# Optimization experiments

Hardware: AMD Instinct MI355X
Metric: run time of the kernel (lower is better)

## Reference

```python
import jax, jax.numpy as jnp
import numpy as np

N = 50000      # nodes
E = 800000     # edges
D_DISC = 64
D_CONT = 13    # per-slice continuous features (39/3)
EMB = 256
HID = 512
SLOPE = 0.01   # torch leaky_relu default


def lrelu(x):
    return jax.nn.leaky_relu(x, SLOPE)


def gcn_conv(x, W, b, src, dst, n):
    """PyG GCNConv with add_self_loops=True (self loops appended by caller),
    symmetric normalization D^-1/2 A D^-1/2, bias."""
    x = x @ W                                   # [N, EMB]
    ones = jnp.ones(src.shape[0], x.dtype)
    deg = jax.ops.segment_sum(ones, dst, num_segments=n)   # in-degree incl self loop
    dinv = jax.lax.rsqrt(jnp.maximum(deg, 1e-12))
    norm = dinv[src] * dinv[dst]                # [E+N]
    out = jax.ops.segment_sum(x[src] * norm[:, None], dst, num_segments=n)
    return out + b


def setup_inputs() -> dict:
    key = jax.random.key(0)
    ks = jax.random.split(key, 24)
    def lin(k, fan_in, fan_out):
        bound = 1.0 / np.sqrt(fan_in)
        k1, k2 = jax.random.split(k)
        W = jax.random.uniform(k1, (fan_in, fan_out), jnp.float32, -bound, bound)
        b = jax.random.uniform(k2, (fan_out,), jnp.float32, -bound, bound)
        return W, b
    Wd, bd = lin(ks[0], D_DISC, EMB)
    Wc1, bc1 = lin(ks[1], D_CONT, EMB)
    Wc2, bc2 = lin(ks[2], D_CONT, EMB)
    Wg0, bg0 = lin(ks[3], D_DISC, EMB)
    Wg1, bg1 = lin(ks[4], EMB, EMB)
    Wg2, bg2 = lin(ks[5], EMB, EMB)
    Wf, bf = lin(ks[6], 4 * EMB, HID)
    Wl1, bl1 = lin(ks[7], HID, HID // 2)
    Wl2, bl2 = lin(ks[8], HID // 2, 1)
    discrete_x = jax.random.normal(ks[9], (N, D_DISC), jnp.float32)
    continous_x = jax.random.normal(ks[10], (N, 3 * D_CONT), jnp.float32)
    edge_index = jax.random.randint(ks[11], (2, E), 0, N, jnp.int64)
    return {
        'discrete_x': discrete_x, 'continous_x': continous_x,
        'Wd': Wd, 'bd': bd, 'Wc1': Wc1, 'bc1': bc1, 'Wc2': Wc2, 'bc2': bc2,
        'Wg0': Wg0, 'bg0': bg0, 'Wg1': Wg1, 'bg1': bg1, 'Wg2': Wg2, 'bg2': bg2,
        'Wf': Wf, 'bf': bf, 'Wl1': Wl1, 'bl1': bl1, 'Wl2': Wl2, 'bl2': bl2,
        'edge_index': edge_index,
    }


def reference(discrete_x, continous_x, Wd, bd, Wc1, bc1, Wc2, bc2,
              Wg0, bg0, Wg1, bg1, Wg2, bg2, Wf, bf, Wl1, bl1, Wl2, bl2,
              edge_index):
    n = discrete_x.shape[0]
    loop = jnp.arange(n, dtype=edge_index.dtype)
    src = jnp.concatenate([edge_index[0], loop])
    dst = jnp.concatenate([edge_index[1], loop])

    x_d = lrelu(discrete_x @ Wd + bd)
    x_c1 = lrelu(continous_x[:, :13] @ Wc1 + bc1)
    x_c2 = lrelu(continous_x[:, 13:26] @ Wc2 + bc2)
    x_g = lrelu(discrete_x @ Wg0 + bg0)
    x_g = lrelu(gcn_conv(x_g, Wg1, bg1, src, dst, n))
    x_g = lrelu(gcn_conv(x_g, Wg2, bg2, src, dst, n))

    h_ci = lrelu(jnp.concatenate([x_d, x_c1, x_c2, x_g], axis=1) @ Wf + bf)
    s = lrelu(h_ci @ Wl1 + bl1)
    # dropout: eval mode (training=False) -> identity
    s_ci = jax.nn.sigmoid((s @ Wl2 + bl2)).squeeze()
    return (s_ci, s_ci, s_ci, h_ci, h_ci)
```

## Files before the change

kernel.cpp:

```cpp
#include <hip/hip_runtime.h>
#include <math.h>

#define NNODES 50000
#define NEDGES 800000
#define EMB 256
#define HID 512


typedef __bf16 bf16x8 __attribute__((ext_vector_type(8)));
typedef float f32x4 __attribute__((ext_vector_type(4)));
typedef unsigned short us4v __attribute__((ext_vector_type(4)));
typedef unsigned short us8v __attribute__((ext_vector_type(8)));

__device__ __forceinline__ unsigned short f2bf(float x) {
    unsigned int u = __float_as_uint(x);
    u += 0x7FFF + ((u >> 16) & 1);
    return (unsigned short)(u >> 16);
}

__device__ __forceinline__ f32x4 mfma_bf16(us8v a, us8v b, f32x4 c) {
    return __builtin_amdgcn_mfma_f32_16x16x32_bf16(
        __builtin_bit_cast(bf16x8, a), __builtin_bit_cast(bf16x8, b), c, 0, 0, 0);
}

__device__ __forceinline__ void gl16(const unsigned short* g, unsigned short* l) {
    __builtin_amdgcn_global_load_lds(
        (const __attribute__((address_space(1))) unsigned int*)g,
        (__attribute__((address_space(3))) unsigned int*)l, 16, 0, 0);
}

__global__ void wsplit(const float* __restrict__ W, int K, int N,
                       unsigned short* __restrict__ th, unsigned short* __restrict__ tl)
{
    int idx = blockIdx.x * 256 + threadIdx.x;
    if (idx >= K * N) return;
    int n = idx / K, k = idx - n * K;
    float x = W[(size_t)k * N + n];
    unsigned short h = f2bf(x);
    float hf = __uint_as_float((unsigned int)h << 16);
    th[idx] = h;
    tl[idx] = f2bf(x - hf);
}

__global__ void xsplit(const float* __restrict__ X, int n,
                       unsigned short* __restrict__ xh, unsigned short* __restrict__ xl)
{
    int i = blockIdx.x * 256 + threadIdx.x;
    if (i >= n) return;
    float x = X[i];
    unsigned short h = f2bf(x);
    xh[i] = h;
    xl[i] = f2bf(x - __uint_as_float((unsigned int)h << 16));
}

__global__ __launch_bounds__(256) void gemm_mfma_p(
    const unsigned short* __restrict__ Ah, const unsigned short* __restrict__ Al, int lda,
    const unsigned short* __restrict__ BTh, const unsigned short* __restrict__ BTl,
    float* __restrict__ C, int ldc, float* __restrict__ C2,
    unsigned short* __restrict__ Ch, unsigned short* __restrict__ Cl, int ldcp,
    const float* __restrict__ bias, int M, int N, int K, int act)
{
    __shared__ unsigned short AsH[2][128 * 64];
    __shared__ unsigned short AsL[2][128 * 64];
    const int bm = blockIdx.y * 128;
    const int bn = blockIdx.x * 128;
    const int tid = threadIdx.x;
    const int lane = tid & 63;
    const int wid = tid >> 6;
    const int wm = wid >> 1, wn = wid & 1;
    const int l15 = lane & 15, l4 = lane >> 4;

    const int rg = lane >> 3;
    const int sb = (lane & 7) ^ rg;
    size_t soff[4];
#pragma unroll
    for (int i = 0; i < 4; ++i) {
        int g = wid * 4 + i;
        soff[i] = (size_t)(bm + g * 8 + rg) * (size_t)lda + (size_t)(sb * 8);
    }

    const unsigned short* bhp[4];
    const unsigned short* blp[4];
#pragma unroll
    for (int fj = 0; fj < 4; ++fj) {
        size_t coff = (size_t)(bn + wn * 64 + fj * 16 + l15) * (size_t)K;
        bhp[fj] = BTh + coff;
        blp[fj] = BTl + coff;
    }

    f32x4 acc[4][4] = {};
    const int nk = K >> 6;

#pragma unroll
    for (int i = 0; i < 4; ++i) {
        int g = wid * 4 + i;
        gl16(Ah + soff[i], &AsH[0][g * 512]);
        gl16(Al + soff[i], &AsL[0][g * 512]);
    }
    __syncthreads();

    for (int t = 0; t < nk; ++t) {
        const int cur = t & 1;
        const int k0 = t * 64;

        us8v bh[2][4], bl[2][4];
#pragma unroll
        for (int ks = 0; ks < 2; ++ks) {
            const size_t kg = (size_t)(k0 + ks * 32 + l4 * 8);
#pragma unroll
            for (int fj = 0; fj < 4; ++fj) {
                bh[ks][fj] = *(const us8v*)(bhp[fj] + kg);
                bl[ks][fj] = *(const us8v*)(blp[fj] + kg);
            }
        }

        if (t + 1 < nk) {
            const size_t ko = (size_t)(k0 + 64);
#pragma unroll
            for (int i = 0; i < 4; ++i) {
                int g = wid * 4 + i;
                gl16(Ah + soff[i] + ko, &AsH[cur ^ 1][g * 512]);
                gl16(Al + soff[i] + ko, &AsL[cur ^ 1][g * 512]);
            }
        }

#pragma unroll
        for (int ks = 0; ks < 2; ++ks) {
            us8v ah[4], al[4];
            const int kb = ks * 4 + l4;
#pragma unroll
            for (int fi = 0; fi < 4; ++fi) {
                int row = wm * 64 + fi * 16 + l15;
                int phys = row * 64 + ((kb ^ (row & 7)) << 3);
                ah[fi] = *(const us8v*)&AsH[cur][phys];
                al[fi] = *(const us8v*)&AsL[cur][phys];
            }
#pragma unroll
            for (int fj = 0; fj < 4; ++fj)
#pragma unroll
                for (int fi = 0; fi < 4; ++fi)
                    acc[fi][fj] = mfma_bf16(ah[fi], bh[ks][fj], acc[fi][fj]);
#pragma unroll
            for (int fj = 0; fj < 4; ++fj)
#pragma unroll
                for (int fi = 0; fi < 4; ++fi)
                    acc[fi][fj] = mfma_bf16(al[fi], bh[ks][fj], acc[fi][fj]);
#pragma unroll
            for (int fj = 0; fj < 4; ++fj)
#pragma unroll
                for (int fi = 0; fi < 4; ++fi)
                    acc[fi][fj] = mfma_bf16(ah[fi], bl[ks][fj], acc[fi][fj]);
        }
        __syncthreads();
    }

    float bs[4];
#pragma unroll
    for (int fj = 0; fj < 4; ++fj)
        bs[fj] = bias ? bias[bn + wn * 64 + fj * 16 + l15] : 0.f;

#pragma unroll
    for (int fi = 0; fi < 4; ++fi) {
#pragma unroll
        for (int r = 0; r < 4; ++r) {
            int row = bm + wm * 64 + fi * 16 + l4 * 4 + r;
            if (row >= M) continue;
#pragma unroll
            for (int fj = 0; fj < 4; ++fj) {
                int col = bn + wn * 64 + fj * 16 + l15;
                float v = acc[fi][fj][r] + bs[fj];
                if (act) v = v > 0.f ? v : 0.01f * v;
                if (C) {
                    C[(size_t)row * ldc + col] = v;
                    if (C2) C2[(size_t)row * ldc + col] = v;
                }
                if (Ch) {
                    unsigned short h = f2bf(v);
                    Ch[(size_t)row * ldcp + col] = h;
                    Cl[(size_t)row * ldcp + col] =
                        f2bf(v - __uint_as_float((unsigned int)h << 16));
                }
            }
        }
    }
}

__global__ __launch_bounds__(256) void gemm_mfma(
    const float* __restrict__ A, int lda,
    const unsigned short* __restrict__ BTh, const unsigned short* __restrict__ BTl,
    float* __restrict__ C, int ldc, float* __restrict__ C2,
    const float* __restrict__ bias, int M, int N, int K, int act)
{
    __shared__ unsigned short AsH[2][128 * 64];
    __shared__ unsigned short AsL[2][128 * 64];
    const int bm = blockIdx.y * 128;
    const int bn = blockIdx.x * 128;
    const int tid = threadIdx.x;
    const int lane = tid & 63;
    const int wid = tid >> 6;
    const int wm = wid >> 1, wn = wid & 1;
    const int l15 = lane & 15, l4 = lane >> 4;

    int smidx[8], sj4[8];
    const float* sptr[8];
#pragma unroll
    for (int u = 0; u < 8; ++u) {
        int fid = tid + u * 256;
        int m = fid >> 4;
        int j4 = fid & 15;
        smidx[u] = m;
        sj4[u] = j4;
        int gr = bm + m;
        sptr[u] = (gr < M) ? (A + (size_t)gr * lda + j4 * 4) : nullptr;
    }

    const unsigned short* bhp[4];
    const unsigned short* blp[4];
#pragma unroll
    for (int fj = 0; fj < 4; ++fj) {
        size_t coff = (size_t)(bn + wn * 64 + fj * 16 + l15) * (size_t)K;
        bhp[fj] = BTh + coff;
        blp[fj] = BTl + coff;
    }

    f32x4 acc[4][4] = {};
    float4 pref[8];
    const int nk = K >> 6;

#pragma unroll
    for (int u = 0; u < 8; ++u)
        pref[u] = sptr[u] ? *(const float4*)(sptr[u]) : make_float4(0.f, 0.f, 0.f, 0.f);

    for (int t = 0; t < nk; ++t) {
        const int cur = t & 1;
#pragma unroll
        for (int u = 0; u < 8; ++u) {
            float e[4] = {pref[u].x, pref[u].y, pref[u].z, pref[u].w};
            us4v h, l;
#pragma unroll
            for (int q = 0; q < 4; ++q) {
                unsigned short hh = f2bf(e[q]);
                h[q] = hh;
                l[q] = f2bf(e[q] - __uint_as_float((unsigned int)hh << 16));
            }
            int m = smidx[u], j4 = sj4[u];
            int phys = m * 64 + ((((j4 >> 1)) ^ (m & 7)) << 3) + (j4 & 1) * 4;
            *(us4v*)&AsH[cur][phys] = h;
            *(us4v*)&AsL[cur][phys] = l;
        }
        __syncthreads();

        if (t + 1 < nk) {
            const int koff = (t + 1) * 64;
#pragma unroll
            for (int u = 0; u < 8; ++u)
                pref[u] = sptr[u] ? *(const float4*)(sptr[u] + koff)
                                  : make_float4(0.f, 0.f, 0.f, 0.f);
        }

        const int k0 = t * 64;
#pragma unroll
        for (int ks = 0; ks < 2; ++ks) {
            us8v ah[4], al[4], bh[4], bl[4];
            const int kb = ks * 4 + l4;
#pragma unroll
            for (int fi = 0; fi < 4; ++fi) {
                int row = wm * 64 + fi * 16 + l15;
                int phys = row * 64 + ((kb ^ (row & 7)) << 3);
                ah[fi] = *(const us8v*)&AsH[cur][phys];
                al[fi] = *(const us8v*)&AsL[cur][phys];
            }
            const size_t kg = (size_t)(k0 + ks * 32 + l4 * 8);
#pragma unroll
            for (int fj = 0; fj < 4; ++fj) {
                bh[fj] = *(const us8v*)(bhp[fj] + kg);
                bl[fj] = *(const us8v*)(blp[fj] + kg);
            }
#pragma unroll
            for (int fj = 0; fj < 4; ++fj)
#pragma unroll
                for (int fi = 0; fi < 4; ++fi)
                    acc[fi][fj] = mfma_bf16(ah[fi], bh[fj], acc[fi][fj]);
#pragma unroll
            for (int fj = 0; fj < 4; ++fj)
#pragma unroll
                for (int fi = 0; fi < 4; ++fi)
                    acc[fi][fj] = mfma_bf16(al[fi], bh[fj], acc[fi][fj]);
#pragma unroll
            for (int fj = 0; fj < 4; ++fj)
#pragma unroll
                for (int fi = 0; fi < 4; ++fi)
                    acc[fi][fj] = mfma_bf16(ah[fi], bl[fj], acc[fi][fj]);
        }
    }

    float bs[4];
#pragma unroll
    for (int fj = 0; fj < 4; ++fj)
        bs[fj] = bias ? bias[bn + wn * 64 + fj * 16 + l15] : 0.f;

#pragma unroll
    for (int fi = 0; fi < 4; ++fi) {
#pragma unroll
        for (int r = 0; r < 4; ++r) {
            int row = bm + wm * 64 + fi * 16 + l4 * 4 + r;
            if (row >= M) continue;
#pragma unroll
            for (int fj = 0; fj < 4; ++fj) {
                int col = bn + wn * 64 + fj * 16 + l15;
                float v = acc[fi][fj][r] + bs[fj];
                if (act) v = v > 0.f ? v : 0.01f * v;
                C[(size_t)row * ldc + col] = v;
                if (C2) C2[(size_t)row * ldc + col] = v;
            }
        }
    }
}

#define BM 128
#define BN 128
#define BK 16

__global__ __launch_bounds__(256) void gemm_kernel(
    const float* __restrict__ A, int lda,
    const float* __restrict__ B, int ldb,
    float* __restrict__ C, int ldc,
    float* __restrict__ C2,
    unsigned short* __restrict__ Ch, unsigned short* __restrict__ Cl, int ldcp,
    const float* __restrict__ bias,
    int M, int N, int K, int act)
{
    __shared__ float As[BK][BM];
    __shared__ float Bs[BK][BN];
    const int bm = blockIdx.y * BM;
    const int bn = blockIdx.x * BN;
    const int tid = threadIdx.x;
    const int tx = tid & 15;
    const int ty = tid >> 4;

    const bool avec = ((((uintptr_t)A) & 15) == 0) && ((lda & 3) == 0);

    float acc[8][8] = {};

    for (int k0 = 0; k0 < K; k0 += BK) {
        if (avec) {
#pragma unroll
            for (int it = 0; it < 2; ++it) {
                int aid = tid + it * 256;
                int m = aid >> 2;
                int kq = aid & 3;
                int gr = bm + m;
                int gk = k0 + kq * 4;
                float4 v = {0.f, 0.f, 0.f, 0.f};
                if (gr < M) {
                    if (gk + 3 < K) {
                        v = *(const float4*)(A + (size_t)gr * lda + gk);
                    } else {
                        float t0 = (gk + 0 < K) ? A[(size_t)gr * lda + gk + 0] : 0.f;
                        float t1 = (gk + 1 < K) ? A[(size_t)gr * lda + gk + 1] : 0.f;
                        float t2 = (gk + 2 < K) ? A[(size_t)gr * lda + gk + 2] : 0.f;
                        float t3 = (gk + 3 < K) ? A[(size_t)gr * lda + gk + 3] : 0.f;
                        v = make_float4(t0, t1, t2, t3);
                    }
                }
                int k = kq * 4;
                As[k + 0][m ^ (((k + 0) & 7) << 2)] = v.x;
                As[k + 1][m ^ (((k + 1) & 7) << 2)] = v.y;
                As[k + 2][m ^ (((k + 2) & 7) << 2)] = v.z;
                As[k + 3][m ^ (((k + 3) & 7) << 2)] = v.w;
            }
        } else {
            for (int l = tid; l < BM * BK; l += 256) {
                int m = l >> 4;
                int k = l & 15;
                int gr = bm + m, gc = k0 + k;
                float v = (gr < M && gc < K) ? A[(size_t)gr * lda + gc] : 0.f;
                As[k][m ^ ((k & 7) << 2)] = v;
            }
        }
#pragma unroll
        for (int it = 0; it < 2; ++it) {
            int fid = tid + it * 256;
            int k = fid >> 5;
            int n4 = fid & 31;
            int gk = k0 + k;
            int gn = bn + n4 * 4;
            float4 v = {0.f, 0.f, 0.f, 0.f};
            if (gk < K) {
                if (gn + 3 < N) {
                    v = *(const float4*)(B + (size_t)gk * ldb + gn);
                } else {
                    float t0 = (gn + 0 < N) ? B[(size_t)gk * ldb + gn + 0] : 0.f;
                    float t1 = (gn + 1 < N) ? B[(size_t)gk * ldb + gn + 1] : 0.f;
                    float t2 = (gn + 2 < N) ? B[(size_t)gk * ldb + gn + 2] : 0.f;
                    float t3 = (gn + 3 < N) ? B[(size_t)gk * ldb + gn + 3] : 0.f;
                    v = make_float4(t0, t1, t2, t3);
                }
            }
            *(float4*)&Bs[k][n4 * 4] = v;
        }
        __syncthreads();

#pragma unroll
        for (int k = 0; k < BK; ++k) {
            const int sw = (k & 7) << 2;
            float4 a0 = *(const float4*)&As[k][(ty * 4) ^ sw];
            float4 a1 = *(const float4*)&As[k][(ty * 4 + 64) ^ sw];
            float4 b0 = *(const float4*)&Bs[k][tx * 4];
            float4 b1 = *(const float4*)&Bs[k][tx * 4 + 64];
            float av[8] = {a0.x, a0.y, a0.z, a0.w, a1.x, a1.y, a1.z, a1.w};
            float bv[8] = {b0.x, b0.y, b0.z, b0.w, b1.x, b1.y, b1.z, b1.w};
#pragma unroll
            for (int i = 0; i < 8; ++i)
#pragma unroll
                for (int j = 0; j < 8; ++j)
                    acc[i][j] += av[i] * bv[j];
        }
        __syncthreads();
    }

#pragma unroll
    for (int i = 0; i < 8; ++i) {
        int r = bm + ((i >> 2) * 64) + ty * 4 + (i & 3);
        if (r >= M) continue;
#pragma unroll
        for (int jh = 0; jh < 2; ++jh) {
            int c0 = bn + jh * 64 + tx * 4;
#pragma unroll
            for (int e = 0; e < 4; ++e) {
                int c = c0 + e;
                if (c >= N) continue;
                float v = acc[i][jh * 4 + e];
                if (bias) v += bias[c];
                if (act) v = v > 0.f ? v : 0.01f * v;
                if (Ch) {
                    unsigned short h = f2bf(v);
                    Ch[(size_t)r * ldcp + c] = h;
                    Cl[(size_t)r * ldcp + c] =
                        f2bf(v - __uint_as_float((unsigned int)h << 16));
                } else {
                    C[(size_t)r * ldc + c] = v;
                    if (C2) C2[(size_t)r * ldc + c] = v;
                }
            }
        }
    }
}

__global__ void count_deg(const int* __restrict__ dst, int* __restrict__ deg, int nE)
{
    int e = blockIdx.x * 256 + threadIdx.x;
    if (e < nE) atomicAdd(&deg[dst[e]], 1);
}

__global__ void dinv_kernel(const int* __restrict__ deg, float* __restrict__ dinv, int n)
{
    int i = blockIdx.x * 256 + threadIdx.x;
    if (i < n) dinv[i] = rsqrtf((float)deg[i] + 1.0f);
}

__global__ __launch_bounds__(256) void scan1(const int* __restrict__ deg,
                                             int* __restrict__ excl,
                                             int* __restrict__ blocksum, int n)
{
    __shared__ int tsum[256];
    int base = blockIdx.x * 1024;
    int t = threadIdx.x;
    int v[4], s = 0;
#pragma unroll
    for (int j = 0; j < 4; ++j) {
        int idx = base + t * 4 + j;
        v[j] = (idx < n) ? deg[idx] : 0;
        s += v[j];
    }
    tsum[t] = s;
    __syncthreads();
    for (int off = 1; off < 256; off <<= 1) {
        int x = (t >= off) ? tsum[t - off] : 0;
        __syncthreads();
        tsum[t] += x;
        __syncthreads();
    }
    int toff = tsum[t] - s;
    int run = 0;
#pragma unroll
    for (int j = 0; j < 4; ++j) {
        int idx = base + t * 4 + j;
        if (idx < n) excl[idx] = toff + run;
        run += v[j];
    }
    if (t == 255) blocksum[blockIdx.x] = tsum[255];
}

__global__ void scan2(int* __restrict__ blocksum, int nb)
{
    if (threadIdx.x == 0 && blockIdx.x == 0) {
        int run = 0;
        for (int i = 0; i < nb; ++i) {
            int v = blocksum[i];
            blocksum[i] = run;
            run += v;
        }
    }
}

__global__ void scan3(int* __restrict__ rowptr, int* __restrict__ cursor,
                      const int* __restrict__ excl, const int* __restrict__ blocksum, int n)
{
    int idx = blockIdx.x * 256 + threadIdx.x;
    if (idx < n) {
        int v = excl[idx] + blocksum[idx >> 10];
        rowptr[idx] = v;
        cursor[idx] = v;
    }
    if (idx == 0) rowptr[n] = NEDGES;
}

__global__ void fill_csr(const int* __restrict__ src, const int* __restrict__ dst,
                         const float* __restrict__ dinv, int* __restrict__ cursor,
                         int* __restrict__ src_sorted, float* __restrict__ w_sorted, int nE)
{
    int e = blockIdx.x * 256 + threadIdx.x;
    if (e >= nE) return;
    int s = src[e], d = dst[e];
    int pos = atomicAdd(&cursor[d], 1);
    src_sorted[pos] = s;
    w_sorted[pos] = dinv[s] * dinv[d];
}

__global__ __launch_bounds__(256) void gather_conv(
    const float* __restrict__ t, const int* __restrict__ rowptr,
    const int* __restrict__ src_sorted, const float* __restrict__ w_sorted,
    const float* __restrict__ dinv, const float* __restrict__ bias,
    unsigned short* __restrict__ oh, unsigned short* __restrict__ ol, int ldcp)
{
    int node = blockIdx.x * 4 + (threadIdx.x >> 6);
    if (node >= NNODES) return;
    int lane = threadIdx.x & 63;
    int p0 = rowptr[node], p1 = rowptr[node + 1];
    const float4* tv = (const float4*)t;
    float4 acc = {0.f, 0.f, 0.f, 0.f};
    for (int p = p0; p < p1; ++p) {
        int s = src_sorted[p];
        float w = w_sorted[p];
        float4 v = tv[(size_t)s * 64 + lane];
        acc.x += v.x * w; acc.y += v.y * w; acc.z += v.z * w; acc.w += v.w * w;
    }
    float di = dinv[node];
    float w2 = di * di;
    float4 self = tv[(size_t)node * 64 + lane];
    float4 b = ((const float4*)bias)[lane];
    float e[4];
    e[0] = acc.x + self.x * w2 + b.x;
    e[1] = acc.y + self.y * w2 + b.y;
    e[2] = acc.z + self.z * w2 + b.z;
    e[3] = acc.w + self.w * w2 + b.w;
    us4v h4, l4v;
#pragma unroll
    for (int q = 0; q < 4; ++q) {
        float v = e[q] > 0.f ? e[q] : 0.01f * e[q];
        unsigned short h = f2bf(v);
        h4[q] = h;
        l4v[q] = f2bf(v - __uint_as_float((unsigned int)h << 16));
    }
    *(us4v*)(oh + (size_t)node * ldcp + lane * 4) = h4;
    *(us4v*)(ol + (size_t)node * ldcp + lane * 4) = l4v;
}

__global__ __launch_bounds__(256) void rowdot_sigmoid(
    const float* __restrict__ s, const float* __restrict__ w, const float* __restrict__ b,
    float* __restrict__ out, int n)
{
    int row = blockIdx.x * 4 + (threadIdx.x >> 6);
    int lane = threadIdx.x & 63;
    if (row >= n) return;
    const float4* sr = (const float4*)(s + (size_t)row * 256);
    const float4* wr = (const float4*)w;
    float4 a = sr[lane], c = wr[lane];
    float p = a.x * c.x + a.y * c.y + a.z * c.z + a.w * c.w;
#pragma unroll
    for (int off = 32; off > 0; off >>= 1) p += __shfl_down(p, off);
    if (lane == 0) {
        float v = 1.0f / (1.0f + expf(-(p + b[0])));
        out[row] = v;
        out[n + row] = v;
        out[2 * n + row] = v;
    }
}

extern "C" void kernel_launch(void* const* d_in, const int* in_sizes, int n_in,
                              void* d_out, int out_size, void* d_ws, size_t ws_size,
                              hipStream_t stream)
{
    const float* discrete_x = (const float*)d_in[0];
    const float* continous_x = (const float*)d_in[1];
    const float* Wd  = (const float*)d_in[2];  const float* bd  = (const float*)d_in[3];
    const float* Wc1 = (const float*)d_in[4];  const float* bc1 = (const float*)d_in[5];
    const float* Wc2 = (const float*)d_in[6];  const float* bc2 = (const float*)d_in[7];
    const float* Wg0 = (const float*)d_in[8];  const float* bg0 = (const float*)d_in[9];
    const float* Wg1 = (const float*)d_in[10]; const float* bg1 = (const float*)d_in[11];
    const float* Wg2 = (const float*)d_in[12]; const float* bg2 = (const float*)d_in[13];
    const float* Wf  = (const float*)d_in[14]; const float* bf  = (const float*)d_in[15];
    const float* Wl1 = (const float*)d_in[16]; const float* bl1 = (const float*)d_in[17];
    const float* Wl2 = (const float*)d_in[18]; const float* bl2 = (const float*)d_in[19];
    const int* edge_index = (const int*)d_in[20];
    const int* src = edge_index;
    const int* dst = edge_index + NEDGES;

    float* out = (float*)d_out;
    float* ws = (float*)d_ws;

    float* dinv       = ws;
    int*   deg        = (int*)(ws + 50048);
    int*   rowptr     = (int*)(ws + 2 * 50048);
    int*   cursor     = (int*)(ws + 3 * 50048 + 64);
    int*   excl       = (int*)(ws + 4 * 50048 + 64);
    int*   blocksum   = (int*)(ws + 5 * 50048 + 64);
    int*   src_sorted = (int*)(ws + 5 * 50048 + 128);
    float* w_sorted   = ws + 5 * 50048 + 128 + NEDGES;
    float* xcat       = w_sorted + NEDGES;
    float* xg         = xcat + (size_t)NNODES * 1024;
    float* tbuf       = xg   + (size_t)NNODES * EMB;
    float* sbuf       = tbuf + (size_t)NNODES * EMB;

    float* h_out  = out + 3 * (size_t)NNODES;
    float* h_out2 = h_out + (size_t)NNODES * HID;

    unsigned short* xcat_h = (unsigned short*)xcat;
    unsigned short* xcat_l = xcat_h + (size_t)NNODES * 1024;
    unsigned short* xg_h   = (unsigned short*)xg;
    unsigned short* xg_l   = xg_h + (size_t)NNODES * 256;

    unsigned short* wl1_h = (unsigned short*)out;
    unsigned short* wl1_l = wl1_h + 512 * 256;
    unsigned short* wd_h  = (unsigned short*)h_out2;
    unsigned short* wd_l  = wd_h  + 64 * 256;
    unsigned short* wg0_h = wd_l  + 64 * 256;
    unsigned short* wg0_l = wg0_h + 64 * 256;
    unsigned short* wg1_h = wg0_l + 64 * 256;
    unsigned short* wg1_l = wg1_h + 256 * 256;
    unsigned short* wg2_h = wg1_l + 256 * 256;
    unsigned short* wg2_l = wg2_h + 256 * 256;
    unsigned short* wf_h  = (unsigned short*)sbuf;
    unsigned short* wf_l  = wf_h + 1024 * 512;
    unsigned short* dx_h  = wf_l + 1024 * 512;
    unsigned short* dx_l  = dx_h + (size_t)NNODES * 64;

    dim3 blk(256);
    auto gemmF = [&](const float* A, int lda, const float* B, int ldb,
                     unsigned short* ch, unsigned short* cl, int ldcp,
                     const float* bias, int M, int N, int K, int act) {
        dim3 grid((N + BN - 1) / BN, (M + BM - 1) / BM);
        hipLaunchKernelGGL(gemm_kernel, grid, blk, 0, stream,
                           A, lda, B, ldb, (float*)nullptr, 0, (float*)nullptr,
                           ch, cl, ldcp, bias, M, N, K, act);
    };
    auto gemmP = [&](const unsigned short* ah, const unsigned short* al, int lda,
                     const unsigned short* th, const unsigned short* tl,
                     float* Cf, int ldc, float* C2,
                     unsigned short* ch, unsigned short* cl, int ldcp,
                     const float* bias, int M, int N, int K, int act) {
        dim3 grid(N / 128, (M + 127) / 128);
        hipLaunchKernelGGL(gemm_mfma_p, grid, blk, 0, stream,
                           ah, al, lda, th, tl, Cf, ldc, C2, ch, cl, ldcp,
                           bias, M, N, K, act);
    };
    auto wsp = [&](const float* W, int K, int N, unsigned short* th, unsigned short* tl) {
        hipLaunchKernelGGL(wsplit, dim3((K * N + 255) / 256), blk, 0, stream, W, K, N, th, tl);
    };

    wsp(Wd,  64,   256, wd_h,  wd_l);
    wsp(Wg0, 64,   256, wg0_h, wg0_l);
    wsp(Wg1, 256,  256, wg1_h, wg1_l);
    wsp(Wg2, 256,  256, wg2_h, wg2_l);
    wsp(Wf,  1024, 512, wf_h,  wf_l);
    wsp(Wl1, 512,  256, wl1_h, wl1_l);
    hipLaunchKernelGGL(xsplit, dim3((NNODES * 64 + 255) / 256), blk, 0, stream,
                       discrete_x, NNODES * 64, dx_h, dx_l);

    hipMemsetAsync(deg, 0, NNODES * sizeof(int), stream);
    hipLaunchKernelGGL(count_deg, dim3((NEDGES + 255) / 256), blk, 0, stream, dst, deg, NEDGES);
    hipLaunchKernelGGL(dinv_kernel, dim3((NNODES + 255) / 256), blk, 0, stream, deg, dinv, NNODES);
    int nb = (NNODES + 1023) / 1024;
    hipLaunchKernelGGL(scan1, dim3(nb), blk, 0, stream, deg, excl, blocksum, NNODES);
    hipLaunchKernelGGL(scan2, dim3(1), blk, 0, stream, blocksum, nb);
    hipLaunchKernelGGL(scan3, dim3((NNODES + 255) / 256), blk, 0, stream,
                       rowptr, cursor, excl, blocksum, NNODES);
    hipLaunchKernelGGL(fill_csr, dim3((NEDGES + 255) / 256), blk, 0, stream,
                       src, dst, dinv, cursor, src_sorted, w_sorted, NEDGES);

    gemmP(dx_h, dx_l, 64, wd_h, wd_l, nullptr, 0, nullptr,
          xcat_h, xcat_l, 1024, bd, NNODES, 256, 64, 1);
    gemmF(continous_x,      39, Wc1, EMB, xcat_h + 256, xcat_l + 256, 1024,
          bc1, NNODES, EMB, 13, 1);
    gemmF(continous_x + 13, 39, Wc2, EMB, xcat_h + 512, xcat_l + 512, 1024,
          bc2, NNODES, EMB, 13, 1);
    gemmP(dx_h, dx_l, 64, wg0_h, wg0_l, nullptr, 0, nullptr,
          xg_h, xg_l, 256, bg0, NNODES, 256, 64, 1);

    gemmP(xg_h, xg_l, 256, wg1_h, wg1_l, tbuf, 256, nullptr,
          nullptr, nullptr, 0, nullptr, NNODES, 256, 256, 0);
    hipLaunchKernelGGL(gather_conv, dim3((NNODES + 3) / 4), blk, 0, stream,
                       tbuf, rowptr, src_sorted, w_sorted, dinv, bg1, xg_h, xg_l, 256);

    gemmP(xg_h, xg_l, 256, wg2_h, wg2_l, tbuf, 256, nullptr,
          nullptr, nullptr, 0, nullptr, NNODES, 256, 256, 0);
    hipLaunchKernelGGL(gather_conv, dim3((NNODES + 3) / 4), blk, 0, stream,
                       tbuf, rowptr, src_sorted, w_sorted, dinv, bg2,
                       xcat_h + 768, xcat_l + 768, 1024);

    gemmP(xcat_h, xcat_l, 1024, wf_h, wf_l, h_out, HID, h_out2,
          nullptr, nullptr, 0, bf, NNODES, 512, 1024, 1);

    {
        dim3 grid(256 / 128, (NNODES + 127) / 128);
        hipLaunchKernelGGL(gemm_mfma, grid, blk, 0, stream,
                           h_out, HID, wl1_h, wl1_l, sbuf, 256, (float*)nullptr,
                           bl1, NNODES, 256, 512, 1);
    }

    hipLaunchKernelGGL(rowdot_sigmoid, dim3((NNODES + 3) / 4), blk, 0, stream,
                       sbuf, Wl2, bl2, out, NNODES);
}
```

Before: 1.302 ms.

## Emit split-bf16 output from fusion GEMM and remap GEMM blocks across XCDs

Measured after the change: 1.288 ms. About the same (-1.0%).

```diff
diff --git a/kernel.cpp b/kernel.cpp
--- a/kernel.cpp
+++ b/kernel.cpp
@@ -62,8 +62,17 @@
 {
     __shared__ unsigned short AsH[2][128 * 64];
     __shared__ unsigned short AsL[2][128 * 64];
-    const int bm = blockIdx.y * 128;
-    const int bn = blockIdx.x * 128;
+
+    const int gx = gridDim.x;
+    const int nwg = gx * gridDim.y;
+    const int hwid = blockIdx.y * gx + blockIdx.x;
+    const int q8 = nwg >> 3, r8 = nwg & 7;
+    const int xcd = hwid & 7, pos = hwid >> 3;
+    const int logical = (xcd < r8) ? (xcd * (q8 + 1) + pos)
+                                   : (r8 * (q8 + 1) + (xcd - r8) * q8 + pos);
+    const int bm = (logical / gx) * 128;
+    const int bn = (logical % gx) * 128;
+
     const int tid = threadIdx.x;
     const int lane = tid & 63;
     const int wid = tid >> 6;
@@ -180,138 +189,6 @@
                     Cl[(size_t)row * ldcp + col] =
                         f2bf(v - __uint_as_float((unsigned int)h << 16));
                 }
-            }
-        }
-    }
-}
-
-__global__ __launch_bounds__(256) void gemm_mfma(
-    const float* __restrict__ A, int lda,
-    const unsigned short* __restrict__ BTh, const unsigned short* __restrict__ BTl,
-    float* __restrict__ C, int ldc, float* __restrict__ C2,
-    const float* __restrict__ bias, int M, int N, int K, int act)
-{
-    __shared__ unsigned short AsH[2][128 * 64];
-    __shared__ unsigned short AsL[2][128 * 64];
-    const int bm = blockIdx.y * 128;
-    const int bn = blockIdx.x * 128;
-    const int tid = threadIdx.x;
-    const int lane = tid & 63;
-    const int wid = tid >> 6;
-    const int wm = wid >> 1, wn = wid & 1;
-    const int l15 = lane & 15, l4 = lane >> 4;
-
-    int smidx[8], sj4[8];
-    const float* sptr[8];
-#pragma unroll
-    for (int u = 0; u < 8; ++u) {
-        int fid = tid + u * 256;
-        int m = fid >> 4;
-        int j4 = fid & 15;
-        smidx[u] = m;
-        sj4[u] = j4;
-        int gr = bm + m;
-        sptr[u] = (gr < M) ? (A + (size_t)gr * lda + j4 * 4) : nullptr;
-    }
-
-    const unsigned short* bhp[4];
-    const unsigned short* blp[4];
-#pragma unroll
-    for (int fj = 0; fj < 4; ++fj) {
-        size_t coff = (size_t)(bn + wn * 64 + fj * 16 + l15) * (size_t)K;
-        bhp[fj] = BTh + coff;
-        blp[fj] = BTl + coff;
-    }
-
-    f32x4 acc[4][4] = {};
-    float4 pref[8];
-    const int nk = K >> 6;
-
-#pragma unroll
-    for (int u = 0; u < 8; ++u)
-        pref[u] = sptr[u] ? *(const float4*)(sptr[u]) : make_float4(0.f, 0.f, 0.f, 0.f);
-
-    for (int t = 0; t < nk; ++t) {
-        const int cur = t & 1;
-#pragma unroll
-        for (int u = 0; u < 8; ++u) {
-            float e[4] = {pref[u].x, pref[u].y, pref[u].z, pref[u].w};
-            us4v h, l;
-#pragma unroll
-            for (int q = 0; q < 4; ++q) {
-                unsigned short hh = f2bf(e[q]);
-                h[q] = hh;
-                l[q] = f2bf(e[q] - __uint_as_float((unsigned int)hh << 16));
-            }
-            int m = smidx[u], j4 = sj4[u];
-            int phys = m * 64 + ((((j4 >> 1)) ^ (m & 7)) << 3) + (j4 & 1) * 4;
-            *(us4v*)&AsH[cur][phys] = h;
-            *(us4v*)&AsL[cur][phys] = l;
-        }
-        __syncthreads();
-
-        if (t + 1 < nk) {
-            const int koff = (t + 1) * 64;
-#pragma unroll
-            for (int u = 0; u < 8; ++u)
-                pref[u] = sptr[u] ? *(const float4*)(sptr[u] + koff)
-                                  : make_float4(0.f, 0.f, 0.f, 0.f);
-        }
-
-        const int k0 = t * 64;
-#pragma unroll
-        for (int ks = 0; ks < 2; ++ks) {
-            us8v ah[4], al[4], bh[4], bl[4];
-            const int kb = ks * 4 + l4;
-#pragma unroll
-            for (int fi = 0; fi < 4; ++fi) {
-                int row = wm * 64 + fi * 16 + l15;
-                int phys = row * 64 + ((kb ^ (row & 7)) << 3);
-                ah[fi] = *(const us8v*)&AsH[cur][phys];
-                al[fi] = *(const us8v*)&AsL[cur][phys];
-            }
-            const size_t kg = (size_t)(k0 + ks * 32 + l4 * 8);
-#pragma unroll
-            for (int fj = 0; fj < 4; ++fj) {
-                bh[fj] = *(const us8v*)(bhp[fj] + kg);
-                bl[fj] = *(const us8v*)(blp[fj] + kg);
-            }
-#pragma unroll
-            for (int fj = 0; fj < 4; ++fj)
-#pragma unroll
-                for (int fi = 0; fi < 4; ++fi)
-                    acc[fi][fj] = mfma_bf16(ah[fi], bh[fj], acc[fi][fj]);
-#pragma unroll
-            for (int fj = 0; fj < 4; ++fj)
-#pragma unroll
-                for (int fi = 0; fi < 4; ++fi)
-                    acc[fi][fj] = mfma_bf16(al[fi], bh[fj], acc[fi][fj]);
-#pragma unroll
-            for (int fj = 0; fj < 4; ++fj)
-#pragma unroll
-                for (int fi = 0; fi < 4; ++fi)
-                    acc[fi][fj] = mfma_bf16(ah[fi], bl[fj], acc[fi][fj]);
-        }
-    }
-
-    float bs[4];
-#pragma unroll
-    for (int fj = 0; fj < 4; ++fj)
-        bs[fj] = bias ? bias[bn + wn * 64 + fj * 16 + l15] : 0.f;
-
-#pragma unroll
-    for (int fi = 0; fi < 4; ++fi) {
-#pragma unroll
-        for (int r = 0; r < 4; ++r) {
-            int row = bm + wm * 64 + fi * 16 + l4 * 4 + r;
-            if (row >= M) continue;
-#pragma unroll
-            for (int fj = 0; fj < 4; ++fj) {
-                int col = bn + wn * 64 + fj * 16 + l15;
-                float v = acc[fi][fj][r] + bs[fj];
-                if (act) v = v > 0.f ? v : 0.01f * v;
-                C[(size_t)row * ldc + col] = v;
-                if (C2) C2[(size_t)row * ldc + col] = v;
             }
         }
     }
@@ -631,6 +508,9 @@
     unsigned short* xg_h   = (unsigned short*)xg;
     unsigned short* xg_l   = xg_h + (size_t)NNODES * 256;
 
+    unsigned short* h_hi = (unsigned short*)xg;
+    unsigned short* h_lo = (unsigned short*)tbuf;
+
     unsigned short* wl1_h = (unsigned short*)out;
     unsigned short* wl1_l = wl1_h + 512 * 256;
     unsigned short* wd_h  = (unsigned short*)h_out2;
@@ -710,14 +590,10 @@
                        xcat_h + 768, xcat_l + 768, 1024);
 
     gemmP(xcat_h, xcat_l, 1024, wf_h, wf_l, h_out, HID, h_out2,
-          nullptr, nullptr, 0, bf, NNODES, 512, 1024, 1);
-
-    {
-        dim3 grid(256 / 128, (NNODES + 127) / 128);
-        hipLaunchKernelGGL(gemm_mfma, grid, blk, 0, stream,
-                           h_out, HID, wl1_h, wl1_l, sbuf, 256, (float*)nullptr,
-                           bl1, NNODES, 256, 512, 1);
-    }
+          h_hi, h_lo, HID, bf, NNODES, 512, 1024, 1);
+
+    gemmP(h_hi, h_lo, HID, wl1_h, wl1_l, sbuf, 256, nullptr,
+          nullptr, nullptr, 0, bl1, NNODES, 256, 512, 1);
 
     hipLaunchKernelGGL(rowdot_sigmoid, dim3((NNODES + 3) / 4), blk, 0, stream,
                        sbuf, Wl2, bl2, out, NNODES);
```
